# Kernel tuning notes

Measured on AMD Instinct MI355X. Metric: run time of the kernel, lower is better.

Reference implementation:

```python
import jax, jax.numpy as jnp
import numpy as np
from jax import lax

D_MODEL = 512
D_STATE = 64
D_CONV = 4
EXPAND = 2
HEADDIM = 64
D_INNER = EXPAND * D_MODEL          # 1024
NHEADS = D_INNER // HEADDIM         # 16
CONV_DIM = D_INNER + 2 * D_STATE    # 1152 (x, B, C go through depthwise conv)
D_PROJ = 2 * D_INNER + 2 * D_STATE + NHEADS  # 2192
EPS = 1e-5


def silu(x):
    return x * jax.nn.sigmoid(x)


def layernorm(x, w, b):
    mu = jnp.mean(x, axis=-1, keepdims=True)
    var = jnp.mean((x - mu) ** 2, axis=-1, keepdims=True)
    return (x - mu) * lax.rsqrt(var + EPS) * w + b


def mamba2(x, in_w, conv_w, conv_b, dt_bias, A_log, D_h, mnorm_w, out_w):
    """Faithful Mamba2 forward (sequential selective-scan form of SSD).
    x: [B, L, D_MODEL]"""
    Bsz, L, _ = x.shape
    zxbcdt = x @ in_w  # [B, L, D_PROJ]
    z = zxbcdt[..., :D_INNER]
    xBC = zxbcdt[..., D_INNER:D_INNER + CONV_DIM]
    dt = zxbcdt[..., -NHEADS:]

    # causal depthwise conv1d over sequence, then SiLU
    xBC_pad = jnp.pad(xBC, ((0, 0), (D_CONV - 1, 0), (0, 0)))
    xBC = lax.conv_general_dilated(
        xBC_pad, conv_w, window_strides=(1,), padding='VALID',
        dimension_numbers=('NWC', 'WIO', 'NWC'), feature_group_count=CONV_DIM)
    xBC = silu(xBC + conv_b)

    xh = xBC[..., :D_INNER].reshape(Bsz, L, NHEADS, HEADDIM)      # [B,L,H,P]
    Bc = xBC[..., D_INNER:D_INNER + D_STATE]                      # [B,L,N]
    Cc = xBC[..., D_INNER + D_STATE:]                             # [B,L,N]

    dt = jax.nn.softplus(dt + dt_bias)          # [B,L,H]
    dA = jnp.exp(dt * (-jnp.exp(A_log)))        # [B,L,H]
    dtx = dt[..., None] * xh                    # [B,L,H,P]

    def step(h, ins):
        dA_t, dtx_t, B_t, C_t = ins  # [B,H], [B,H,P], [B,N], [B,N]
        h = h * dA_t[:, :, None, None] + dtx_t[..., None] * B_t[:, None, None, :]
        y = jnp.einsum('bhpn,bn->bhp', h, C_t)
        return h, y

    h0 = jnp.zeros((Bsz, NHEADS, HEADDIM, D_STATE), x.dtype)
    xs = (jnp.moveaxis(dA, 1, 0), jnp.moveaxis(dtx, 1, 0),
          jnp.moveaxis(Bc, 1, 0), jnp.moveaxis(Cc, 1, 0))
    _, ys = lax.scan(step, h0, xs)              # [L,B,H,P]
    y = jnp.moveaxis(ys, 0, 1) + D_h[None, None, :, None] * xh
    y = y.reshape(Bsz, L, D_INNER)

    # gated RMSNorm: rmsnorm(y * silu(z)) * weight
    g = y * silu(z)
    g = g * lax.rsqrt(jnp.mean(g * g, axis=-1, keepdims=True) + EPS) * mnorm_w
    return g @ out_w  # [B, L, D_MODEL]


def setup_inputs() -> dict:
    key = jax.random.key(0)
    ks = jax.random.split(key, 16)
    B, L = 2, 4096
    s = 0.02
    inp = {
        'x': jax.random.normal(ks[0], (B, L, D_MODEL), jnp.float32),
        'norm_in_w': jnp.ones((D_MODEL,), jnp.float32),
        'norm_in_b': jnp.zeros((D_MODEL,), jnp.float32),
        'norm_out_w': jnp.ones((D_MODEL,), jnp.float32),
        'norm_out_b': jnp.zeros((D_MODEL,), jnp.float32),
        'in_w': jax.random.normal(ks[1], (D_MODEL, D_PROJ), jnp.float32) * s,
        'conv_w': jax.random.normal(ks[2], (D_CONV, 1, CONV_DIM), jnp.float32) * 0.1,
        'conv_b': jnp.zeros((CONV_DIM,), jnp.float32),
        'dt_bias': jnp.log(jnp.expm1(jax.random.uniform(ks[3], (NHEADS,), jnp.float32, 0.001, 0.1))),
        'A_log': jnp.log(jnp.arange(1, NHEADS + 1, dtype=jnp.float32)),
        'D_h': jnp.ones((NHEADS,), jnp.float32),
        'mnorm_w': jnp.ones((D_INNER,), jnp.float32),
        'out_w': jax.random.normal(ks[4], (D_INNER, D_MODEL), jnp.float32) * s,
        'ff_w1': jax.random.normal(ks[5], (D_MODEL, 4 * D_MODEL), jnp.float32) * s,
        'ff_b1': jnp.zeros((4 * D_MODEL,), jnp.float32),
        'ff_w2': jax.random.normal(ks[6], (4 * D_MODEL, D_MODEL), jnp.float32) * s,
        'ff_b2': jnp.zeros((D_MODEL,), jnp.float32),
    }
    return inp


def reference(x, norm_in_w, norm_in_b, norm_out_w, norm_out_b, in_w, conv_w,
              conv_b, dt_bias, A_log, D_h, mnorm_w, out_w, ff_w1, ff_b1,
              ff_w2, ff_b2):
    xn = layernorm(x, norm_in_w, norm_in_b)
    fwd = mamba2(xn, in_w, conv_w, conv_b, dt_bias, A_log, D_h, mnorm_w, out_w)
    bwd = mamba2(jnp.flip(xn, axis=1), in_w, conv_w, conv_b, dt_bias, A_log,
                 D_h, mnorm_w, out_w)
    m = layernorm(fwd + jnp.flip(bwd, axis=1), norm_out_w, norm_out_b)
    ff = jax.nn.gelu(m @ ff_w1 + ff_b1, approximate=False) @ ff_w2 + ff_b2
    return ff + x
```

## Files before the change

### kernel.cpp

```cpp
#include <hip/hip_runtime.h>
#include <hip/hip_bf16.h>

#define LSEQ 4096
#define BSZ 2
#define DMODEL 512
#define DINNER 1024
#define DSTATE 64
#define NHEADS 16
#define CONVDIM 1152
#define DPROJ 2192
#define NPAD 2304
#define NTOK (BSZ*LSEQ)
#define NCH 64

typedef __attribute__((ext_vector_type(8))) short short8;
typedef __attribute__((ext_vector_type(4))) float f32x4;

__device__ inline unsigned short f2b(float v){
  unsigned int u = __builtin_bit_cast(unsigned int, v);
  unsigned int r = (u + 0x7FFFu + ((u >> 16) & 1u)) >> 16;
  return (unsigned short)r;
}
__device__ inline float b2f(unsigned short u){
  unsigned int x = ((unsigned int)u) << 16;
  return __builtin_bit_cast(float, x);
}
__device__ inline uint4 pack8(const float* v){
  uint4 pk;
  pk.x = (unsigned)f2b(v[0]) | ((unsigned)f2b(v[1])<<16);
  pk.y = (unsigned)f2b(v[2]) | ((unsigned)f2b(v[3])<<16);
  pk.z = (unsigned)f2b(v[4]) | ((unsigned)f2b(v[5])<<16);
  pk.w = (unsigned)f2b(v[6]) | ((unsigned)f2b(v[7])<<16);
  return pk;
}
__device__ inline float gelu_f(float x){
  float x2 = x*x;
  float u = x*(0.7978845608f + 0.0356774081f*x2);
  float au = fabsf(u);
  float z = __expf(-2.f*au);
  float t = (1.f - z)/(1.f + z);
  t = (u >= 0.f) ? t : -t;
  return 0.5f*x*(1.f + t);
}

#define GLL16(gp, lp) __builtin_amdgcn_global_load_lds( \
    (const __attribute__((address_space(1))) unsigned int*)(gp), \
    (__attribute__((address_space(3))) unsigned int*)(lp), 16, 0, 0)

__global__ __launch_bounds__(256) void wconv_t(const float* __restrict__ src,
    unsigned short* __restrict__ dst, int K, int Nsrc, int Npad){
  __shared__ float t[32][33];
  int n0 = blockIdx.x*32, k0 = blockIdx.y*32;
  int tx = threadIdx.x & 31, ty = threadIdx.x >> 5;
  for (int i=0;i<4;i++){
    int k = k0 + ty + i*8; int n = n0 + tx;
    t[ty + i*8][tx] = (n < Nsrc) ? src[(size_t)k*Nsrc + n] : 0.f;
  }
  __syncthreads();
  for (int i=0;i<4;i++){
    int n = n0 + ty + i*8; int k = k0 + tx;
    if (n < Npad) dst[(size_t)n*K + k] = f2b(t[tx][ty + i*8]);
  }
}

__global__ __launch_bounds__(256) void layernorm_k(const float* __restrict__ in,
    const float* __restrict__ w, const float* __restrict__ bb, unsigned short* __restrict__ out){
  int row = blockIdx.x; int tid = threadIdx.x;
  const float* r = in + (size_t)row*DMODEL;
  float v0 = r[tid], v1 = r[tid+256];
  float s = v0+v1, sq = v0*v0+v1*v1;
  for (int m=32;m>=1;m>>=1){ s += __shfl_xor(s,m); sq += __shfl_xor(sq,m); }
  __shared__ float ws_[4], wq_[4];
  int wave = tid>>6, lane = tid&63;
  if (lane==0){ ws_[wave]=s; wq_[wave]=sq; }
  __syncthreads();
  s = ws_[0]+ws_[1]+ws_[2]+ws_[3]; sq = wq_[0]+wq_[1]+wq_[2]+wq_[3];
  float mu = s * (1.f/DMODEL);
  float var = sq * (1.f/DMODEL) - mu*mu;
  float rs = rsqrtf(var + 1e-5f);
  out[(size_t)row*DMODEL + tid]     = f2b((v0-mu)*rs*w[tid] + bb[tid]);
  out[(size_t)row*DMODEL + tid+256] = f2b((v1-mu)*rs*w[tid+256] + bb[tid+256]);
}

__global__ __launch_bounds__(256) void layernorm2_k(const float* __restrict__ in0,
    const float* __restrict__ in1,
    const float* __restrict__ w, const float* __restrict__ bb, unsigned short* __restrict__ out){
  int row = blockIdx.x; int tid = threadIdx.x;
  const float* r0 = in0 + (size_t)row*DMODEL;
  const float* r1 = in1 + (size_t)row*DMODEL;
  float v0 = r0[tid] + r1[tid], v1 = r0[tid+256] + r1[tid+256];
  float s = v0+v1, sq = v0*v0+v1*v1;
  for (int m=32;m>=1;m>>=1){ s += __shfl_xor(s,m); sq += __shfl_xor(sq,m); }
  __shared__ float ws_[4], wq_[4];
  int wave = tid>>6, lane = tid&63;
  if (lane==0){ ws_[wave]=s; wq_[wave]=sq; }
  __syncthreads();
  s = ws_[0]+ws_[1]+ws_[2]+ws_[3]; sq = wq_[0]+wq_[1]+wq_[2]+wq_[3];
  float mu = s * (1.f/DMODEL);
  float var = sq * (1.f/DMODEL) - mu*mu;
  float rs = rsqrtf(var + 1e-5f);
  out[(size_t)row*DMODEL + tid]     = f2b((v0-mu)*rs*w[tid] + bb[tid]);
  out[(size_t)row*DMODEL + tid+256] = f2b((v1-mu)*rs*w[tid+256] + bb[tid+256]);
}

__global__ __launch_bounds__(256) void reduce4_k(const float* __restrict__ pa,
    const float* __restrict__ pb, const float* __restrict__ bias,
    const float* __restrict__ resid, float* __restrict__ out){
  const size_t MN4 = (size_t)NTOK*DMODEL/4;
  for (size_t i = (size_t)blockIdx.x*256 + threadIdx.x; i < MN4; i += (size_t)gridDim.x*256){
    float4 a0 = ((const float4*)pa)[i];
    float4 a1 = ((const float4*)pa)[i + MN4];
    float4 b0 = ((const float4*)pb)[i];
    float4 b1 = ((const float4*)pb)[i + MN4];
    float4 rv = ((const float4*)resid)[i];
    int col = (int)((i*4) & (DMODEL-1));
    const float4 bs = *(const float4*)(bias + col);
    float4 o;
    o.x = a0.x + a1.x + b0.x + b1.x + bs.x + rv.x;
    o.y = a0.y + a1.y + b0.y + b1.y + bs.y + rv.y;
    o.z = a0.z + a1.z + b0.z + b1.z + bs.z + rv.z;
    o.w = a0.w + a1.w + b0.w + b1.w + bs.w + rv.w;
    ((float4*)out)[i] = o;
  }
}

__global__ __launch_bounds__(512, 2) void gemm256_k(const unsigned short* __restrict__ A,
    const unsigned short* __restrict__ Bt, void* __restrict__ outp, void* __restrict__ outp_hi,
    int M, int N, int K, int klen, int epi, const float* __restrict__ bias){
  __shared__ __align__(16) unsigned short As[32768];
  __shared__ __align__(16) unsigned short Bs[32768];
  const int tid = threadIdx.x;
  const int lane = tid & 63, wave = tid >> 6;
  const int wr = wave >> 2, wc = wave & 3;
  const int l15 = lane & 15, q = lane >> 4;
  int nbx = gridDim.x;
  int bid = blockIdx.y * nbx + blockIdx.x;
  int cpx = (nbx * gridDim.y) >> 3;
  int swz = (bid & 7) * cpx + (bid >> 3);
  int bn = swz % nbx, bm = swz / nbx;
  const int kstart = blockIdx.z * klen;
  const int NT = klen >> 6;
  const int j0 = tid, j1 = tid + 512;
  const int rr0 = j0 >> 2, rr1 = j1 >> 2;
  const int sc0 = (j0 & 3) ^ ((rr0 >> 1) & 3);
  const int sc1 = (j1 & 3) ^ ((rr1 >> 1) & 3);
  const unsigned short* a0 = A  + (size_t)(bm*256 + rr0)*K + kstart + sc0*8;
  const unsigned short* a1 = A  + (size_t)(bm*256 + rr1)*K + kstart + sc1*8;
  const unsigned short* b0 = Bt + (size_t)(bn*256 + rr0)*K + kstart + sc0*8;
  const unsigned short* b1 = Bt + (size_t)(bn*256 + rr1)*K + kstart + sc1*8;
  unsigned short* lA0 = As + j0*8;
  unsigned short* lA1 = As + j1*8;
  unsigned short* lB0 = Bs + j0*8;
  unsigned short* lB1 = Bs + j1*8;
#define STGA(t,kh) { const int go=(t)*64+(kh)*32, lo=((t)&1)*16384+(kh)*8192; \
  GLL16(a0+go, lA0+lo); GLL16(a1+go, lA1+lo); }
#define STGB(t,kh) { const int go=(t)*64+(kh)*32, lo=((t)&1)*16384+(kh)*8192; \
  GLL16(b0+go, lB0+lo); GLL16(b1+go, lB1+lo); }
  f32x4 acc[8][4];
  #pragma unroll
  for (int i=0;i<8;i++)
    #pragma unroll
    for (int j=0;j<4;j++) acc[i][j] = (f32x4){0.f,0.f,0.f,0.f};
  STGA(0,0); STGB(0,0); STGA(0,1); STGB(0,1);
  STGA(1,0); STGB(1,0);
  asm volatile("s_waitcnt vmcnt(4)" ::: "memory");
  __builtin_amdgcn_s_barrier();
  const int cOfs = (q ^ ((l15 >> 1) & 3)) * 8;
  const int arow = wr*128 + l15;
  const int brow = wc*64  + l15;
  for (int t = 0; t < NT; ++t){
    const unsigned short* Ab = As + (t & 1)*16384;
    const unsigned short* Bb = Bs + (t & 1)*16384;
    short8 af[4], bf4[4];
    #pragma unroll
    for (int mi=0;mi<4;mi++) af[mi]  = *(const short8*)(Ab + (arow + mi*16)*32 + cOfs);
    #pragma unroll
    for (int nt=0;nt<4;nt++) bf4[nt] = *(const short8*)(Bb + (brow + nt*16)*32 + cOfs);
    if (t+1 < NT) STGA(t+1,1);
    __builtin_amdgcn_s_barrier();
    asm volatile("s_waitcnt lgkmcnt(0)" ::: "memory");
    __builtin_amdgcn_sched_barrier(0);
    __builtin_amdgcn_s_setprio(1);
    #pragma unroll
    for (int mi=0;mi<4;mi++)
      #pragma unroll
      for (int nt=0;nt<4;nt++)
        acc[mi][nt] = __builtin_amdgcn_mfma_f32_16x16x32_bf16(af[mi], bf4[nt], acc[mi][nt], 0,0,0);
    __builtin_amdgcn_s_setprio(0);
    __builtin_amdgcn_s_barrier();
    #pragma unroll
    for (int mi=0;mi<4;mi++) af[mi] = *(const short8*)(Ab + (arow + (4+mi)*16)*32 + cOfs);
    if (t+1 < NT) STGB(t+1,1);
    __builtin_amdgcn_s_barrier();
    asm volatile("s_waitcnt lgkmcnt(0)" ::: "memory");
    __builtin_amdgcn_sched_barrier(0);
    __builtin_amdgcn_s_setprio(1);
    #pragma unroll
    for (int mi=0;mi<4;mi++)
      #pragma unroll
      for (int nt=0;nt<4;nt++)
        acc[4+mi][nt] = __builtin_amdgcn_mfma_f32_16x16x32_bf16(af[mi], bf4[nt], acc[4+mi][nt], 0,0,0);
    __builtin_amdgcn_s_setprio(0);
    __builtin_amdgcn_s_barrier();
    #pragma unroll
    for (int mi=0;mi<4;mi++) af[mi]  = *(const short8*)(Ab + 8192 + (arow + mi*16)*32 + cOfs);
    #pragma unroll
    for (int nt=0;nt<4;nt++) bf4[nt] = *(const short8*)(Bb + 8192 + (brow + nt*16)*32 + cOfs);
    if (t+2 < NT) STGA(t+2,0);
    __builtin_amdgcn_s_barrier();
    asm volatile("s_waitcnt lgkmcnt(0)" ::: "memory");
    __builtin_amdgcn_sched_barrier(0);
    __builtin_amdgcn_s_setprio(1);
    #pragma unroll
    for (int mi=0;mi<4;mi++)
      #pragma unroll
      for (int nt=0;nt<4;nt++)
        acc[mi][nt] = __builtin_amdgcn_mfma_f32_16x16x32_bf16(af[mi], bf4[nt], acc[mi][nt], 0,0,0);
    __builtin_amdgcn_s_setprio(0);
    __builtin_amdgcn_s_barrier();
    #pragma unroll
    for (int mi=0;mi<4;mi++) af[mi] = *(const short8*)(Ab + 8192 + (arow + (4+mi)*16)*32 + cOfs);
    if (t+2 < NT) STGB(t+2,0);
    __builtin_amdgcn_s_barrier();
    asm volatile("s_waitcnt lgkmcnt(0)" ::: "memory");
    __builtin_amdgcn_sched_barrier(0);
    __builtin_amdgcn_s_setprio(1);
    #pragma unroll
    for (int mi=0;mi<4;mi++)
      #pragma unroll
      for (int nt=0;nt<4;nt++)
        acc[4+mi][nt] = __builtin_amdgcn_mfma_f32_16x16x32_bf16(af[mi], bf4[nt], acc[4+mi][nt], 0,0,0);
    __builtin_amdgcn_s_setprio(0);
    if (t+2 < NT)      { asm volatile("s_waitcnt vmcnt(4)" ::: "memory"); }
    else if (t+1 < NT) { asm volatile("s_waitcnt vmcnt(0)" ::: "memory"); }
    __builtin_amdgcn_s_barrier();
  }
#undef STGA
#undef STGB
  float* cb = (float*)As + wave*1040;
  const int rbase = q*4;
  const int gr0t = bm*256 + wr*128;
  const int gc0 = bn*256 + wc*64;
  #pragma unroll
  for (int mt=0; mt<8; mt++){
    #pragma unroll
    for (int nt=0;nt<4;nt++)
      #pragma unroll
      for (int r=0;r<4;r++)
        cb[(rbase+r)*65 + nt*16 + l15] = acc[mt][nt][r];
    int gr0 = gr0t + mt*16;
    if (epi == 0){
      float* po = (float*)((blockIdx.z < 2) ? outp : outp_hi)
                + (size_t)(blockIdx.z & 1) * ((size_t)M * N);
      int r4 = lane >> 4, c0f = (lane & 15)*4;
      #pragma unroll
      for (int h=0; h<4; h++){
        int row = h*4 + r4;
        float4 v;
        v.x = cb[row*65 + c0f + 0];
        v.y = cb[row*65 + c0f + 1];
        v.z = cb[row*65 + c0f + 2];
        v.w = cb[row*65 + c0f + 3];
        *(float4*)(po + (size_t)(gr0+row)*N + gc0 + c0f) = v;
      }
    } else {
      int r8 = lane >> 3, c0 = (lane & 7)*8;
      #pragma unroll
      for (int h=0; h<2; h++){
        int row = h*8 + r8;
        float v[8];
        #pragma unroll
        for (int u=0;u<8;u++) v[u] = cb[row*65 + c0 + u];
        if (epi == 1){
          #pragma unroll
          for (int u=0;u<8;u++) v[u] = gelu_f(v[u] + bias[gc0 + c0 + u]);
        }
        *(uint4*)((unsigned short*)outp + (size_t)(gr0+row)*N + gc0 + c0) = pack8(v);
      }
    }
  }
}

__global__ __launch_bounds__(256) void dt_k(const unsigned short* __restrict__ zx,
    const float* __restrict__ dt_bias, const float* __restrict__ A_log,
    float* __restrict__ dAb, float* __restrict__ dtb){
  int b = blockIdx.y;
  int t = blockIdx.x*16 + (threadIdx.x>>4);
  int h = threadIdx.x & 15;
  float raw = b2f(zx[((size_t)b*LSEQ + t)*NPAD + (DINNER+CONVDIM) + h]) + dt_bias[h];
  float dt = (raw > 20.f) ? raw : log1pf(expf(raw));
  float dA = expf(-expf(A_log[h]) * dt);
  size_t f = ((size_t)b*LSEQ + t)*NHEADS + h;
  size_t r = ((size_t)(BSZ+b)*LSEQ + (LSEQ-1-t))*NHEADS + h;
  dAb[f] = dA; dtb[f] = dt;
  dAb[r] = dA; dtb[r] = dt;
}

__global__ __launch_bounds__(256) void conv_x_k(const unsigned short* __restrict__ zx,
    const float* __restrict__ conv_w, const float* __restrict__ conv_b,
    const float* __restrict__ dtb, unsigned short* __restrict__ dtxb,
    unsigned short* __restrict__ zcomp){
  int b = blockIdx.y;
  int t0blk = blockIdx.x * 32;
  int tid = threadIdx.x;
  int half = tid >> 7, cg = tid & 127;
  int c0 = cg * 8;
  int head = c0 >> 6;
  float wk[4][8], bias8[8];
  #pragma unroll
  for (int k=0;k<4;k++)
    #pragma unroll
    for (int j=0;j<8;j++) wk[k][j] = conv_w[k*CONVDIM + c0 + j];
  #pragma unroll
  for (int j=0;j<8;j++) bias8[j] = conv_b[c0 + j];
  __shared__ float sdtf[32][16], sdtb[32][16];
  for (int r = tid; r < 512; r += 256){
    int i = r >> 4, h = r & 15;
    sdtf[i][h] = dtb[((size_t)b*LSEQ + t0blk + i)*NHEADS + h];
    sdtb[i][h] = dtb[((size_t)(BSZ+b)*LSEQ + (LSEQ-1-(t0blk+i)))*NHEADS + h];
  }
  __syncthreads();
  int t0 = t0blk + half*16;
  float w0[8],w1[8],w2[8],w3[8];
  #pragma unroll
  for (int j=0;j<8;j++){ w1[j]=0.f; w2[j]=0.f; w3[j]=0.f; }
  for (int it=0; it<22; ++it){
    int t = t0 - 3 + it;
    #pragma unroll
    for (int j=0;j<8;j++){ w0[j]=w1[j]; w1[j]=w2[j]; w2[j]=w3[j]; }
    if (t >= 0 && t < LSEQ){
      uint4 xv = *(const uint4*)(zx + ((size_t)b*LSEQ + t)*NPAD + DINNER + c0);
      const unsigned short* xs = (const unsigned short*)&xv;
      #pragma unroll
      for (int j=0;j<8;j++) w3[j] = b2f(xs[j]);
      if (t >= t0 && t < t0+16){
        uint4 zv = *(const uint4*)(zx + ((size_t)b*LSEQ + t)*NPAD + c0);
        *(uint4*)(zcomp + ((size_t)b*LSEQ + t)*DINNER + c0) = zv;
      }
    } else {
      #pragma unroll
      for (int j=0;j<8;j++) w3[j] = 0.f;
    }
    if (t >= t0 && t < t0+16){
      float dtf = sdtf[t - t0blk][head];
      float v[8];
      #pragma unroll
      for (int j=0;j<8;j++){
        float a = bias8[j] + wk[0][j]*w0[j] + wk[1][j]*w1[j] + wk[2][j]*w2[j] + wk[3][j]*w3[j];
        v[j] = (a / (1.f + __expf(-a))) * dtf;
      }
      *(uint4*)(dtxb + ((size_t)b*LSEQ + t)*DINNER + c0) = pack8(v);
    }
    int tau = t - 3;
    if (tau >= t0 && tau < t0+16){
      float dtv = sdtb[tau - t0blk][head];
      float v[8];
      #pragma unroll
      for (int j=0;j<8;j++){
        float a = bias8[j] + wk[0][j]*w3[j] + wk[1][j]*w2[j] + wk[2][j]*w1[j] + wk[3][j]*w0[j];
        v[j] = (a / (1.f + __expf(-a))) * dtv;
      }
      *(uint4*)(dtxb + ((size_t)(BSZ+b)*LSEQ + (LSEQ-1-tau))*DINNER + c0) = pack8(v);
    }
  }
}

__global__ __launch_bounds__(256) void conv_bc_k(const unsigned short* __restrict__ zx,
    const float* __restrict__ conv_w, const float* __restrict__ conv_b,
    unsigned short* __restrict__ Bb, unsigned short* __restrict__ Cb){
  int b = blockIdx.y;
  int t0blk = blockIdx.x * 64;
  int tid = threadIdx.x;
  int slot = tid >> 4, cg = tid & 15;
  int c0 = cg*8;
  int ccol = DINNER + 1024 + c0;
  int cw = 1024 + c0;
  float wk[4][8], bias8[8];
  #pragma unroll
  for (int k=0;k<4;k++)
    #pragma unroll
    for (int j=0;j<8;j++) wk[k][j] = conv_w[k*CONVDIM + cw + j];
  #pragma unroll
  for (int j=0;j<8;j++) bias8[j] = conv_b[cw + j];
  int t0 = t0blk + slot*4;
  float w0[8],w1[8],w2[8],w3[8];
  #pragma unroll
  for (int j=0;j<8;j++){ w1[j]=0.f; w2[j]=0.f; w3[j]=0.f; }
  for (int it=0; it<10; ++it){
    int t = t0 - 3 + it;
    #pragma unroll
    for (int j=0;j<8;j++){ w0[j]=w1[j]; w1[j]=w2[j]; w2[j]=w3[j]; }
    if (t >= 0 && t < LSEQ){
      uint4 xv = *(const uint4*)(zx + ((size_t)b*LSEQ + t)*NPAD + ccol);
      const unsigned short* xs = (const unsigned short*)&xv;
      #pragma unroll
      for (int j=0;j<8;j++) w3[j] = b2f(xs[j]);
    } else {
      #pragma unroll
      for (int j=0;j<8;j++) w3[j] = 0.f;
    }
    if (t >= t0 && t < t0+4){
      float v[8];
      #pragma unroll
      for (int j=0;j<8;j++){
        float a = bias8[j] + wk[0][j]*w0[j] + wk[1][j]*w1[j] + wk[2][j]*w2[j] + wk[3][j]*w3[j];
        v[j] = a / (1.f + __expf(-a));
      }
      size_t tok = (size_t)b*LSEQ + t;
      if (c0 < 64) *(uint4*)(Bb + tok*DSTATE + c0)      = pack8(v);
      else         *(uint4*)(Cb + tok*DSTATE + (c0-64)) = pack8(v);
    }
    int tau = t - 3;
    if (tau >= t0 && tau < t0+4){
      float v[8];
      #pragma unroll
      for (int j=0;j<8;j++){
        float a = bias8[j] + wk[0][j]*w3[j] + wk[1][j]*w2[j] + wk[2][j]*w1[j] + wk[3][j]*w0[j];
        v[j] = a / (1.f + __expf(-a));
      }
      size_t tok = (size_t)(BSZ+b)*LSEQ + (LSEQ-1-tau);
      if (c0 < 64) *(uint4*)(Bb + tok*DSTATE + c0)      = pack8(v);
      else         *(uint4*)(Cb + tok*DSTATE + (c0-64)) = pack8(v);
    }
  }
}

template<int SA, int SB>
__device__ inline void gemm64s(const unsigned short* Ab, const unsigned short* Bb_,
                               int l15, int q, f32x4 acc[4][4]){
  #pragma unroll
  for (int ks=0; ks<2; ks++){
    short8 af[4], bf4[4];
    #pragma unroll
    for (int mt=0;mt<4;mt++){
      int r = mt*16 + l15;
      int c = ks*4 + q; if (SA) c ^= (r>>3)&7;
      af[mt] = *(const short8*)(Ab + r*72 + c*8);
    }
    #pragma unroll
    for (int nt=0;nt<4;nt++){
      int r = nt*16 + l15;
      int c = ks*4 + q; if (SB) c ^= (r>>3)&7;
      bf4[nt] = *(const short8*)(Bb_ + r*72 + c*8);
    }
    #pragma unroll
    for (int mt=0;mt<4;mt++)
      #pragma unroll
      for (int nt=0;nt<4;nt++)
        acc[mt][nt] = __builtin_amdgcn_mfma_f32_16x16x32_bf16(af[mt], bf4[nt], acc[mt][nt], 0,0,0);
  }
}
__device__ inline void gemm64(const unsigned short* Ab, const unsigned short* Bb_,
                              int l15, int q, f32x4 acc[4][4]){
  gemm64s<0,0>(Ab, Bb_, l15, q, acc);
}

__global__ __launch_bounds__(64) void ssd1_k(const float* __restrict__ dAb,
    const unsigned short* __restrict__ dtxb, const unsigned short* __restrict__ Bb,
    const unsigned short* __restrict__ Cb,
    unsigned short* __restrict__ y0, unsigned short* __restrict__ y1,
    unsigned short* __restrict__ hbuf, float* __restrict__ Pch, float* __restrict__ ebuf){
  int ch = blockIdx.x, h = blockIdx.y, z = blockIdx.z;
  int d = z >> 1, b = z & 1;
  int lane = threadIdx.x;
  int l15 = lane & 15, q = lane >> 4;
  int tr = lane >> 3, cb8 = (lane & 7)*8;
  int m7 = lane & 7;
  size_t tokb = (size_t)z*LSEQ + (size_t)ch*64;
  size_t zhc = ((size_t)z*NHEADS + h)*NCH + ch;
  __shared__ __align__(16) unsigned short S1[64*72];
  __shared__ __align__(16) unsigned short S2[64*72];
  __shared__ __align__(16) unsigned short S3[64*72];
  __shared__ float Lb[64];
  float L = fmaxf(logf(dAb[(tokb + lane)*NHEADS + h]), -60.f);
  #pragma unroll
  for (int off=1; off<64; off<<=1){
    float v = __shfl_up(L, off);
    if (lane >= off) L += v;
  }
  Lb[lane] = L;
  float e = __expf(L);
  ebuf[zhc*64 + lane] = e;
  if (lane == 63) Pch[zhc] = e;
  for (int i=0;i<8;i++){
    int t = i*8 + tr;
    *(uint4*)&S1[t*72 + cb8] = *(const uint4*)(Cb + (tokb+t)*DSTATE + cb8);
    *(uint4*)&S2[t*72 + cb8] = *(const uint4*)(Bb + (tokb+t)*DSTATE + cb8);
    uint4 xv = *(const uint4*)(dtxb + (tokb+t)*DINNER + (size_t)h*64 + cb8);
    const unsigned short* xs = (const unsigned short*)&xv;
    int csw = ((i ^ m7) << 3) + tr;
    #pragma unroll
    for (int j=0;j<8;j++) S3[(cb8+j)*72 + csw] = xs[j];
  }
  f32x4 sa[4][4];
  for (int i=0;i<4;i++) for (int j=0;j<4;j++) sa[i][j] = (f32x4){0.f,0.f,0.f,0.f};
  gemm64s<0,0>(S1, S2, l15, q, sa);
  float Lsv[4];
  #pragma unroll
  for (int nt=0;nt<4;nt++) Lsv[nt] = Lb[nt*16 + l15];
  int sch = l15 >> 3, sin = l15 & 7;
  #pragma unroll
  for (int mt=0;mt<4;mt++){
    #pragma unroll
    for (int r=0;r<4;r++){
      int t = mt*16 + q*4 + r;
      int trow = (t>>3)&7;
      float Lt = Lb[t];
      #pragma unroll
      for (int nt=0;nt<4;nt++){
        int s = nt*16 + l15;
        float v = (t >= s) ? __expf(Lt - Lsv[nt]) * sa[mt][nt][r] : 0.f;
        S1[t*72 + (((nt*2 + sch) ^ trow)<<3) + sin] = f2b(v);
      }
    }
  }
  f32x4 ya[4][4];
  for (int i=0;i<4;i++) for (int j=0;j<4;j++) ya[i][j] = (f32x4){0.f,0.f,0.f,0.f};
  gemm64s<1,1>(S1, S3, l15, q, ya);
  #pragma unroll
  for (int mt=0;mt<4;mt++)
    #pragma unroll
    for (int pt=0;pt<4;pt++)
      #pragma unroll
      for (int r=0;r<4;r++)
        S2[(mt*16+q*4+r)*72 + pt*16 + l15] = f2b(ya[mt][pt][r]);
  unsigned short* yb = d ? y1 : y0;
  for (int i=0;i<8;i++){
    int t = i*8 + tr; int g = ch*64 + t;
    int tph = d ? (LSEQ-1-g) : g;
    *(uint4*)(yb + ((size_t)b*LSEQ + tph)*DINNER + (size_t)h*64 + cb8) = *(uint4*)&S2[t*72 + cb8];
  }
  float L63 = Lb[63];
  for (int i=0;i<8;i++){
    int s = i*8 + tr;
    float w = __expf(L63 - Lb[s]);
    uint4 bv = *(const uint4*)(Bb + (tokb+s)*DSTATE + cb8);
    const unsigned short* bs = (const unsigned short*)&bv;
    int csw = ((i ^ m7) << 3) + tr;
    #pragma unroll
    for (int j=0;j<8;j++) S2[(cb8+j)*72 + csw] = f2b(w * b2f(bs[j]));
  }
  f32x4 ga[4][4];
  for (int i=0;i<4;i++) for (int j=0;j<4;j++) ga[i][j] = (f32x4){0.f,0.f,0.f,0.f};
  gemm64s<1,1>(S3, S2, l15, q, ga);
  #pragma unroll
  for (int pt=0;pt<4;pt++)
    #pragma unroll
    for (int nt=0;nt<4;nt++)
      #pragma unroll
      for (int r=0;r<4;r++)
        S1[(pt*16+q*4+r)*72 + nt*16 + l15] = f2b(ga[pt][nt][r]);
  for (int i=0;i<8;i++){
    int p = i*8 + tr;
    *(uint4*)(hbuf + zhc*4096 + (size_t)p*64 + cb8) = *(uint4*)&S1[p*72 + cb8];
  }
}

__global__ __launch_bounds__(256) void comb_k(unsigned short* __restrict__ hbuf,
    const float* __restrict__ Pch){
  int u = blockIdx.x; int tid = threadIdx.x;
  int kb = blockIdx.y * 4;
  size_t base0 = ((size_t)u*NCH)*4096;
  float hreg[4];
  unsigned short ccur[4], cnxt[4] = {0,0,0,0};
  #pragma unroll
  for (int k=0;k<4;k++){ hreg[k]=0.f; ccur[k] = hbuf[base0 + tid + (size_t)(kb+k)*256]; }
  float Pc = Pch[(size_t)u*NCH], Pn = 0.f;
  for (int ch=0; ch<NCH; ch++){
    size_t base = base0 + (size_t)ch*4096;
    if (ch+1 < NCH){
      size_t bnx = base + 4096;
      #pragma unroll
      for (int k=0;k<4;k++) cnxt[k] = hbuf[bnx + tid + (size_t)(kb+k)*256];
      Pn = Pch[(size_t)u*NCH + ch + 1];
    }
    #pragma unroll
    for (int k=0;k<4;k++){
      hbuf[base + tid + (size_t)(kb+k)*256] = f2b(hreg[k]);
      hreg[k] = hreg[k]*Pc + b2f(ccur[k]);
    }
    #pragma unroll
    for (int k=0;k<4;k++) ccur[k] = cnxt[k];
    Pc = Pn;
  }
}

__global__ __launch_bounds__(64) void ssd2_k(const unsigned short* __restrict__ Cb,
    const unsigned short* __restrict__ hbuf, const unsigned short* __restrict__ dtxb,
    const float* __restrict__ dtb, const float* __restrict__ ebuf, const float* __restrict__ Dh,
    unsigned short* __restrict__ y0, unsigned short* __restrict__ y1){
  int ch = blockIdx.x, h = blockIdx.y, z = blockIdx.z;
  int d = z >> 1, b = z & 1;
  int lane = threadIdx.x;
  int l15 = lane & 15, q = lane >> 4;
  int tr = lane >> 3, cb8 = (lane & 7)*8;
  size_t tokb = (size_t)z*LSEQ + (size_t)ch*64;
  size_t zhc = ((size_t)z*NHEADS + h)*NCH + ch;
  __shared__ __align__(16) unsigned short S1[64*72];
  __shared__ __align__(16) unsigned short S2[64*72];
  __shared__ __align__(16) unsigned short S3[64*72];
  __shared__ float eb2[64], dti[64];
  eb2[lane] = ebuf[zhc*64 + lane];
  dti[lane] = 1.f / dtb[(tokb + lane)*NHEADS + h];
  float Dv = Dh[h];
  for (int i=0;i<8;i++){
    int t = i*8 + tr;
    *(uint4*)&S1[t*72 + cb8] = *(const uint4*)(Cb + (tokb+t)*DSTATE + cb8);
    *(uint4*)&S2[t*72 + cb8] = *(const uint4*)(hbuf + zhc*4096 + (size_t)t*64 + cb8);
  }
  f32x4 acc[4][4];
  for (int i=0;i<4;i++) for (int j=0;j<4;j++) acc[i][j] = (f32x4){0.f,0.f,0.f,0.f};
  gemm64(S1, S2, l15, q, acc);
  unsigned short* yb = d ? y1 : y0;
  #pragma unroll
  for (int mt=0;mt<4;mt++){
    #pragma unroll
    for (int r=0;r<4;r++){
      int t = mt*16 + q*4 + r; int g = ch*64 + t;
      int tph = d ? (LSEQ-1-g) : g;
      size_t rowb = ((size_t)b*LSEQ + tph)*DINNER + (size_t)h*64;
      size_t dxb_ = (tokb + t)*DINNER + (size_t)h*64;
      float et = eb2[t], di = dti[t];
      #pragma unroll
      for (int pt=0;pt<4;pt++){
        int p = pt*16 + l15;
        float v = acc[mt][pt][r]*et + b2f(yb[rowb + p]) + Dv * b2f(dtxb[dxb_ + p]) * di;
        S3[t*72 + p] = f2b(v);
      }
    }
  }
  for (int i=0;i<8;i++){
    int t = i*8 + tr; int g = ch*64 + t;
    int tph = d ? (LSEQ-1-g) : g;
    *(uint4*)(yb + ((size_t)b*LSEQ + tph)*DINNER + (size_t)h*64 + cb8) = *(uint4*)&S3[t*72 + cb8];
  }
}

__global__ __launch_bounds__(256) void gate_k(const unsigned short* __restrict__ y0,
    const unsigned short* __restrict__ y1, const unsigned short* __restrict__ zcomp,
    const float* __restrict__ mnw, unsigned short* __restrict__ gsum){
  int tok = blockIdx.x; int tid = threadIdx.x;
  __shared__ float g0s[DINNER], g1s[DINNER];
  float ss0 = 0.f, ss1 = 0.f;
  for (int i=0;i<4;i++){
    int c = tid + i*256;
    float z = b2f(zcomp[(size_t)tok*DINNER + c]);
    float sz = z / (1.f + __expf(-z));
    float g0 = b2f(y0[(size_t)tok*DINNER + c]) * sz;
    float g1 = b2f(y1[(size_t)tok*DINNER + c]) * sz;
    g0s[c] = g0; g1s[c] = g1;
    ss0 += g0*g0; ss1 += g1*g1;
  }
  for (int m=32;m>=1;m>>=1){ ss0 += __shfl_xor(ss0,m); ss1 += __shfl_xor(ss1,m); }
  __shared__ float w0[4], w1[4];
  int wave = tid>>6, lane = tid&63;
  if (lane==0){ w0[wave]=ss0; w1[wave]=ss1; }
  __syncthreads();
  ss0 = w0[0]+w0[1]+w0[2]+w0[3];
  ss1 = w1[0]+w1[1]+w1[2]+w1[3];
  float r0 = rsqrtf(ss0*(1.f/DINNER) + 1e-5f);
  float r1 = rsqrtf(ss1*(1.f/DINNER) + 1e-5f);
  for (int i=0;i<4;i++){
    int c = tid + i*256;
    gsum[(size_t)tok*DINNER + c] = f2b((g0s[c]*r0 + g1s[c]*r1) * mnw[c]);
  }
}

extern "C" void kernel_launch(void* const* d_in, const int* in_sizes, int n_in,
                              void* d_out, int out_size, void* d_ws, size_t ws_size,
                              hipStream_t stream){
  const float* x       = (const float*)d_in[0];
  const float* nin_w   = (const float*)d_in[1];
  const float* nin_b   = (const float*)d_in[2];
  const float* nout_w  = (const float*)d_in[3];
  const float* nout_b  = (const float*)d_in[4];
  const float* in_w    = (const float*)d_in[5];
  const float* conv_w  = (const float*)d_in[6];
  const float* conv_b  = (const float*)d_in[7];
  const float* dt_bias = (const float*)d_in[8];
  const float* A_log   = (const float*)d_in[9];
  const float* D_h     = (const float*)d_in[10];
  const float* mnorm_w = (const float*)d_in[11];
  const float* out_w   = (const float*)d_in[12];
  const float* ff_w1   = (const float*)d_in[13];
  const float* ff_b1   = (const float*)d_in[14];
  const float* ff_w2   = (const float*)d_in[15];
  const float* ff_b2   = (const float*)d_in[16];
  float* out = (float*)d_out;

  char* ws = (char*)d_ws;
  size_t off = 0;
  auto alloc = [&](size_t bytes)->char*{
    char* p = ws + off; off = (off + bytes + 255) & ~(size_t)255; return p; };
  unsigned short* xn_bf = (unsigned short*)alloc((size_t)NTOK*DMODEL*2);
  unsigned short* in_wT = (unsigned short*)alloc((size_t)NPAD*DMODEL*2);
  unsigned short* out_wT= (unsigned short*)alloc((size_t)DMODEL*DINNER*2);
  unsigned short* w1T   = (unsigned short*)alloc((size_t)2048*DMODEL*2);
  unsigned short* w2T   = (unsigned short*)alloc((size_t)DMODEL*2048*2);
  unsigned short* zx    = (unsigned short*)alloc((size_t)NTOK*NPAD*2);
  unsigned short* zcomp = (unsigned short*)alloc((size_t)NTOK*DINNER*2);
  float*          dAb   = (float*)alloc((size_t)2*NTOK*NHEADS*4);
  float*          dtb   = (float*)alloc((size_t)2*NTOK*NHEADS*4);
  unsigned short* Bb    = (unsigned short*)alloc((size_t)2*NTOK*DSTATE*2);
  unsigned short* Cb    = (unsigned short*)alloc((size_t)2*NTOK*DSTATE*2);
  unsigned short* dtxb  = (unsigned short*)alloc((size_t)2*NTOK*DINNER*2);
  unsigned short* y0    = (unsigned short*)alloc((size_t)NTOK*DINNER*2);
  unsigned short* y1    = (unsigned short*)alloc((size_t)NTOK*DINNER*2);
  float*          Pch   = (float*)alloc((size_t)64*NCH*4);
  float*          ebuf  = (float*)alloc((size_t)64*NCH*64*4);
  size_t need = off;
  if (need > ws_size) return;

  unsigned short* hbuf  = zx;
  unsigned short* gsum  = dtxb;
  unsigned short* m_bf  = y0;
  unsigned short* h1    = zx;
  float* mp   = (float*)zx;
  float* fp01 = (float*)dtxb;
  float* fp23 = (float*)y0;

  wconv_t<<<dim3(NPAD/32,   DMODEL/32), 256, 0, stream>>>(in_w,  in_wT,  DMODEL, DPROJ,  NPAD);
  wconv_t<<<dim3(DMODEL/32, DINNER/32), 256, 0, stream>>>(out_w, out_wT, DINNER, DMODEL, DMODEL);
  wconv_t<<<dim3(2048/32,   DMODEL/32), 256, 0, stream>>>(ff_w1, w1T,    DMODEL, 2048,   2048);
  wconv_t<<<dim3(DMODEL/32, 2048/32),   256, 0, stream>>>(ff_w2, w2T,    2048,   DMODEL, DMODEL);
  layernorm_k<<<NTOK, 256, 0, stream>>>(x, nin_w, nin_b, xn_bf);
  gemm256_k<<<dim3(NPAD/256, NTOK/256, 1), 512, 0, stream>>>(xn_bf, in_wT, zx, nullptr, NTOK, NPAD, DMODEL, DMODEL, 3, nullptr);
  dt_k<<<dim3(LSEQ/16, BSZ), 256, 0, stream>>>(zx, dt_bias, A_log, dAb, dtb);
  conv_x_k<<<dim3(LSEQ/32, BSZ), 256, 0, stream>>>(zx, conv_w, conv_b, dtb, dtxb, zcomp);
  conv_bc_k<<<dim3(LSEQ/64, BSZ), 256, 0, stream>>>(zx, conv_w, conv_b, Bb, Cb);
  ssd1_k<<<dim3(NCH, NHEADS, 2*BSZ), 64, 0, stream>>>(dAb, dtxb, Bb, Cb, y0, y1, hbuf, Pch, ebuf);
  comb_k<<<dim3(64, 4), 256, 0, stream>>>(hbuf, Pch);
  ssd2_k<<<dim3(NCH, NHEADS, 2*BSZ), 64, 0, stream>>>(Cb, hbuf, dtxb, dtb, ebuf, D_h, y0, y1);
  gate_k<<<NTOK, 256, 0, stream>>>(y0, y1, zcomp, mnorm_w, gsum);
  gemm256_k<<<dim3(DMODEL/256, NTOK/256, 2), 512, 0, stream>>>(gsum, out_wT, mp, nullptr, NTOK, DMODEL, DINNER, 512, 0, nullptr);
  layernorm2_k<<<NTOK, 256, 0, stream>>>(mp, mp + (size_t)NTOK*DMODEL, nout_w, nout_b, m_bf);
  gemm256_k<<<dim3(2048/256, NTOK/256, 1), 512, 0, stream>>>(m_bf, w1T, h1, nullptr, NTOK, 2048, DMODEL, DMODEL, 1, ff_b1);
  gemm256_k<<<dim3(DMODEL/256, NTOK/256, 4), 512, 0, stream>>>(h1, w2T, fp01, fp23, NTOK, DMODEL, 2048, 512, 0, nullptr);
  reduce4_k<<<2048, 256, 0, stream>>>(fp01, fp23, ff_b2, x, out);
}
```

Measured before the change: 403.1 us.

## Software-pipeline LDS fragment loads with register double-buffering in GEMM main loop

Restructures the bf16 MFMA GEMM inner loop so LDS fragment reads for the next quarter-step go into separate register buffers (a0f/a1f/b0f/b1f) while the current MFMAs run. Most per-quarter barriers and explicit lgkmcnt(0) waits are removed, and the first fragments of the next k-tile are prefetched right after the end-of-iteration barrier. The aim is to hide LDS latency and cut synchronisation stalls. In exchange it raises register pressure and changes the vmcnt bookkeeping, which risks races on the double-buffered LDS tiles or lower occupancy.

```diff
diff --git a/kernel.cpp b/kernel.cpp
--- a/kernel.cpp
+++ b/kernel.cpp
@@ -165,71 +165,70 @@
   STGA(1,0); STGB(1,0);
   asm volatile("s_waitcnt vmcnt(4)" ::: "memory");
   __builtin_amdgcn_s_barrier();
+  __builtin_amdgcn_sched_barrier(0);
   const int cOfs = (q ^ ((l15 >> 1) & 3)) * 8;
   const int arow = wr*128 + l15;
   const int brow = wc*64  + l15;
+  short8 a0f[4], a1f[4], b0f[4], b1f[4];
+  #pragma unroll
+  for (int mi=0;mi<4;mi++) a0f[mi] = *(const short8*)(As + (arow + mi*16)*32 + cOfs);
+  #pragma unroll
+  for (int nt=0;nt<4;nt++) b0f[nt] = *(const short8*)(Bs + (brow + nt*16)*32 + cOfs);
   for (int t = 0; t < NT; ++t){
-    const unsigned short* Ab = As + (t & 1)*16384;
-    const unsigned short* Bb = Bs + (t & 1)*16384;
-    short8 af[4], bf4[4];
-    #pragma unroll
-    for (int mi=0;mi<4;mi++) af[mi]  = *(const short8*)(Ab + (arow + mi*16)*32 + cOfs);
-    #pragma unroll
-    for (int nt=0;nt<4;nt++) bf4[nt] = *(const short8*)(Bb + (brow + nt*16)*32 + cOfs);
+    const unsigned short* Ab  = As + (t & 1)*16384;
+    const unsigned short* Bb  = Bs + (t & 1)*16384;
+    const unsigned short* Abn = As + ((~t) & 1)*16384;
+    const unsigned short* Bbn = Bs + ((~t) & 1)*16384;
+    #pragma unroll
+    for (int mi=0;mi<4;mi++) a1f[mi] = *(const short8*)(Ab + (arow + (4+mi)*16)*32 + cOfs);
     if (t+1 < NT) STGA(t+1,1);
-    __builtin_amdgcn_s_barrier();
-    asm volatile("s_waitcnt lgkmcnt(0)" ::: "memory");
-    __builtin_amdgcn_sched_barrier(0);
     __builtin_amdgcn_s_setprio(1);
     #pragma unroll
     for (int mi=0;mi<4;mi++)
       #pragma unroll
       for (int nt=0;nt<4;nt++)
-        acc[mi][nt] = __builtin_amdgcn_mfma_f32_16x16x32_bf16(af[mi], bf4[nt], acc[mi][nt], 0,0,0);
+        acc[mi][nt] = __builtin_amdgcn_mfma_f32_16x16x32_bf16(a0f[mi], b0f[nt], acc[mi][nt], 0,0,0);
+    __builtin_amdgcn_s_setprio(0);
+    #pragma unroll
+    for (int mi=0;mi<4;mi++) a0f[mi] = *(const short8*)(Ab + 8192 + (arow + mi*16)*32 + cOfs);
+    #pragma unroll
+    for (int nt=0;nt<4;nt++) b1f[nt] = *(const short8*)(Bb + 8192 + (brow + nt*16)*32 + cOfs);
+    if (t+1 < NT) STGB(t+1,1);
+    __builtin_amdgcn_s_setprio(1);
+    #pragma unroll
+    for (int mi=0;mi<4;mi++)
+      #pragma unroll
+      for (int nt=0;nt<4;nt++)
+        acc[4+mi][nt] = __builtin_amdgcn_mfma_f32_16x16x32_bf16(a1f[mi], b0f[nt], acc[4+mi][nt], 0,0,0);
     __builtin_amdgcn_s_setprio(0);
     __builtin_amdgcn_s_barrier();
     #pragma unroll
-    for (int mi=0;mi<4;mi++) af[mi] = *(const short8*)(Ab + (arow + (4+mi)*16)*32 + cOfs);
-    if (t+1 < NT) STGB(t+1,1);
+    for (int mi=0;mi<4;mi++) a1f[mi] = *(const short8*)(Ab + 8192 + (arow + (4+mi)*16)*32 + cOfs);
+    if (t+2 < NT) STGA(t+2,0);
+    __builtin_amdgcn_s_setprio(1);
+    #pragma unroll
+    for (int mi=0;mi<4;mi++)
+      #pragma unroll
+      for (int nt=0;nt<4;nt++)
+        acc[mi][nt] = __builtin_amdgcn_mfma_f32_16x16x32_bf16(a0f[mi], b1f[nt], acc[mi][nt], 0,0,0);
+    __builtin_amdgcn_s_setprio(0);
+    if (t+2 < NT) STGB(t+2,0);
+    if (t+2 < NT)      { asm volatile("s_waitcnt vmcnt(8)" ::: "memory"); }
+    else if (t+1 < NT) { asm volatile("s_waitcnt vmcnt(4)" ::: "memory"); }
     __builtin_amdgcn_s_barrier();
-    asm volatile("s_waitcnt lgkmcnt(0)" ::: "memory");
     __builtin_amdgcn_sched_barrier(0);
+    if (t+1 < NT){
+      #pragma unroll
+      for (int mi=0;mi<4;mi++) a0f[mi] = *(const short8*)(Abn + (arow + mi*16)*32 + cOfs);
+      #pragma unroll
+      for (int nt=0;nt<4;nt++) b0f[nt] = *(const short8*)(Bbn + (brow + nt*16)*32 + cOfs);
+    }
     __builtin_amdgcn_s_setprio(1);
     #pragma unroll
     for (int mi=0;mi<4;mi++)
       #pragma unroll
       for (int nt=0;nt<4;nt++)
-        acc[4+mi][nt] = __builtin_amdgcn_mfma_f32_16x16x32_bf16(af[mi], bf4[nt], acc[4+mi][nt], 0,0,0);
-    __builtin_amdgcn_s_setprio(0);
-    __builtin_amdgcn_s_barrier();
-    #pragma unroll
-    for (int mi=0;mi<4;mi++) af[mi]  = *(const short8*)(Ab + 8192 + (arow + mi*16)*32 + cOfs);
-    #pragma unroll
-    for (int nt=0;nt<4;nt++) bf4[nt] = *(const short8*)(Bb + 8192 + (brow + nt*16)*32 + cOfs);
-    if (t+2 < NT) STGA(t+2,0);
-    __builtin_amdgcn_s_barrier();
-    asm volatile("s_waitcnt lgkmcnt(0)" ::: "memory");
-    __builtin_amdgcn_sched_barrier(0);
-    __builtin_amdgcn_s_setprio(1);
-    #pragma unroll
-    for (int mi=0;mi<4;mi++)
-      #pragma unroll
-      for (int nt=0;nt<4;nt++)
-        acc[mi][nt] = __builtin_amdgcn_mfma_f32_16x16x32_bf16(af[mi], bf4[nt], acc[mi][nt], 0,0,0);
-    __builtin_amdgcn_s_setprio(0);
-    __builtin_amdgcn_s_barrier();
-    #pragma unroll
-    for (int mi=0;mi<4;mi++) af[mi] = *(const short8*)(Ab + 8192 + (arow + (4+mi)*16)*32 + cOfs);
-    if (t+2 < NT) STGB(t+2,0);
-    __builtin_amdgcn_s_barrier();
-    asm volatile("s_waitcnt lgkmcnt(0)" ::: "memory");
-    __builtin_amdgcn_sched_barrier(0);
-    __builtin_amdgcn_s_setprio(1);
-    #pragma unroll
-    for (int mi=0;mi<4;mi++)
-      #pragma unroll
-      for (int nt=0;nt<4;nt++)
-        acc[4+mi][nt] = __builtin_amdgcn_mfma_f32_16x16x32_bf16(af[mi], bf4[nt], acc[4+mi][nt], 0,0,0);
+        acc[4+mi][nt] = __builtin_amdgcn_mfma_f32_16x16x32_bf16(a1f[mi], b1f[nt], acc[4+mi][nt], 0,0,0);
     __builtin_amdgcn_s_setprio(0);
     if (t+2 < NT)      { asm volatile("s_waitcnt vmcnt(4)" ::: "memory"); }
     else if (t+1 < NT) { asm volatile("s_waitcnt vmcnt(0)" ::: "memory"); }
```

Result: no change. 403.7 us (+0.2%).

## Shrink GEMM tile to 128x256 with simpler double-buffered K=32 pipeline

Applied to the files above, without the earlier changes.

Replaces the 256x256 GEMM kernel with a 128x256 tile that steps K by 32, uses a single-stage double-buffered load per iteration and a smaller LDS footprint, and raises launch bounds to allow more resident blocks. All four GEMMs now launch twice as many blocks. The out-projection GEMM switches to a 4-way split-K, so its layernorm now sums four partials. The aim is better occupancy and more blocks to fill the GPU's CUs, at the cost of less data reuse per tile and more frequent barriers.

```diff
diff --git a/kernel.cpp b/kernel.cpp
--- a/kernel.cpp
+++ b/kernel.cpp
@@ -82,13 +82,13 @@
   out[(size_t)row*DMODEL + tid+256] = f2b((v1-mu)*rs*w[tid+256] + bb[tid+256]);
 }
 
-__global__ __launch_bounds__(256) void layernorm2_k(const float* __restrict__ in0,
-    const float* __restrict__ in1,
+__global__ __launch_bounds__(256) void layernorm4_k(const float* __restrict__ in0,
+    const float* __restrict__ in1, const float* __restrict__ in2, const float* __restrict__ in3,
     const float* __restrict__ w, const float* __restrict__ bb, unsigned short* __restrict__ out){
   int row = blockIdx.x; int tid = threadIdx.x;
-  const float* r0 = in0 + (size_t)row*DMODEL;
-  const float* r1 = in1 + (size_t)row*DMODEL;
-  float v0 = r0[tid] + r1[tid], v1 = r0[tid+256] + r1[tid+256];
+  size_t o = (size_t)row*DMODEL;
+  float v0 = in0[o+tid] + in1[o+tid] + in2[o+tid] + in3[o+tid];
+  float v1 = in0[o+tid+256] + in1[o+tid+256] + in2[o+tid+256] + in3[o+tid+256];
   float s = v0+v1, sq = v0*v0+v1*v1;
   for (int m=32;m>=1;m>>=1){ s += __shfl_xor(s,m); sq += __shfl_xor(sq,m); }
   __shared__ float ws_[4], wq_[4];
@@ -99,8 +99,8 @@
   float mu = s * (1.f/DMODEL);
   float var = sq * (1.f/DMODEL) - mu*mu;
   float rs = rsqrtf(var + 1e-5f);
-  out[(size_t)row*DMODEL + tid]     = f2b((v0-mu)*rs*w[tid] + bb[tid]);
-  out[(size_t)row*DMODEL + tid+256] = f2b((v1-mu)*rs*w[tid+256] + bb[tid+256]);
+  out[o + tid]     = f2b((v0-mu)*rs*w[tid] + bb[tid]);
+  out[o + tid+256] = f2b((v1-mu)*rs*w[tid+256] + bb[tid+256]);
 }
 
 __global__ __launch_bounds__(256) void reduce4_k(const float* __restrict__ pa,
@@ -124,11 +124,12 @@
   }
 }
 
-__global__ __launch_bounds__(512, 2) void gemm256_k(const unsigned short* __restrict__ A,
+__global__ __launch_bounds__(512, 4) void gemm128_k(const unsigned short* __restrict__ A,
     const unsigned short* __restrict__ Bt, void* __restrict__ outp, void* __restrict__ outp_hi,
     int M, int N, int K, int klen, int epi, const float* __restrict__ bias){
-  __shared__ __align__(16) unsigned short As[32768];
-  __shared__ __align__(16) unsigned short Bs[32768];
+  __shared__ __align__(16) unsigned short sm[24576];
+  unsigned short* As = sm;
+  unsigned short* Bs = sm + 8192;
   const int tid = threadIdx.x;
   const int lane = tid & 63, wave = tid >> 6;
   const int wr = wave >> 2, wc = wave & 3;
@@ -139,110 +140,57 @@
   int swz = (bid & 7) * cpx + (bid >> 3);
   int bn = swz % nbx, bm = swz / nbx;
   const int kstart = blockIdx.z * klen;
-  const int NT = klen >> 6;
-  const int j0 = tid, j1 = tid + 512;
-  const int rr0 = j0 >> 2, rr1 = j1 >> 2;
-  const int sc0 = (j0 & 3) ^ ((rr0 >> 1) & 3);
-  const int sc1 = (j1 & 3) ^ ((rr1 >> 1) & 3);
-  const unsigned short* a0 = A  + (size_t)(bm*256 + rr0)*K + kstart + sc0*8;
-  const unsigned short* a1 = A  + (size_t)(bm*256 + rr1)*K + kstart + sc1*8;
-  const unsigned short* b0 = Bt + (size_t)(bn*256 + rr0)*K + kstart + sc0*8;
-  const unsigned short* b1 = Bt + (size_t)(bn*256 + rr1)*K + kstart + sc1*8;
-  unsigned short* lA0 = As + j0*8;
-  unsigned short* lA1 = As + j1*8;
-  unsigned short* lB0 = Bs + j0*8;
-  unsigned short* lB1 = Bs + j1*8;
-#define STGA(t,kh) { const int go=(t)*64+(kh)*32, lo=((t)&1)*16384+(kh)*8192; \
-  GLL16(a0+go, lA0+lo); GLL16(a1+go, lA1+lo); }
-#define STGB(t,kh) { const int go=(t)*64+(kh)*32, lo=((t)&1)*16384+(kh)*8192; \
-  GLL16(b0+go, lB0+lo); GLL16(b1+go, lB1+lo); }
-  f32x4 acc[8][4];
-  #pragma unroll
-  for (int i=0;i<8;i++)
+  const int NT = klen >> 5;
+  const int ra  = tid >> 2;
+  const int sca = (tid & 3) ^ ((ra >> 1) & 3);
+  const int jb1 = tid + 512;
+  const int rb1 = jb1 >> 2;
+  const int scb1 = (jb1 & 3) ^ ((rb1 >> 1) & 3);
+  const unsigned short* ga  = A  + (size_t)(bm*128 + ra )*K + kstart + sca*8;
+  const unsigned short* gb0 = Bt + (size_t)(bn*256 + ra )*K + kstart + sca*8;
+  const unsigned short* gb1 = Bt + (size_t)(bn*256 + rb1)*K + kstart + scb1*8;
+  unsigned short* lAa = As + tid*8;
+  unsigned short* lB0 = Bs + tid*8;
+  unsigned short* lB1 = Bs + jb1*8;
+#define STG(t) { const int go=(t)*32, loa=((t)&1)*4096, lob=((t)&1)*8192; \
+  GLL16(ga+go, lAa+loa); GLL16(gb0+go, lB0+lob); GLL16(gb1+go, lB1+lob); }
+  f32x4 acc[4][4];
+  #pragma unroll
+  for (int i=0;i<4;i++)
     #pragma unroll
     for (int j=0;j<4;j++) acc[i][j] = (f32x4){0.f,0.f,0.f,0.f};
-  STGA(0,0); STGB(0,0); STGA(0,1); STGB(0,1);
-  STGA(1,0); STGB(1,0);
-  asm volatile("s_waitcnt vmcnt(4)" ::: "memory");
-  __builtin_amdgcn_s_barrier();
+  STG(0); STG(1);
   const int cOfs = (q ^ ((l15 >> 1) & 3)) * 8;
-  const int arow = wr*128 + l15;
-  const int brow = wc*64  + l15;
+  const int arow = wr*64 + l15;
+  const int brow = wc*64 + l15;
   for (int t = 0; t < NT; ++t){
-    const unsigned short* Ab = As + (t & 1)*16384;
-    const unsigned short* Bb = Bs + (t & 1)*16384;
+    if (t+1 < NT) { asm volatile("s_waitcnt vmcnt(3)" ::: "memory"); }
+    else          { asm volatile("s_waitcnt vmcnt(0)" ::: "memory"); }
+    __builtin_amdgcn_s_barrier();
+    const unsigned short* Ab = As + (t & 1)*4096;
+    const unsigned short* Bb = Bs + (t & 1)*8192;
     short8 af[4], bf4[4];
     #pragma unroll
-    for (int mi=0;mi<4;mi++) af[mi]  = *(const short8*)(Ab + (arow + mi*16)*32 + cOfs);
+    for (int mt=0;mt<4;mt++) af[mt]  = *(const short8*)(Ab + (arow + mt*16)*32 + cOfs);
     #pragma unroll
     for (int nt=0;nt<4;nt++) bf4[nt] = *(const short8*)(Bb + (brow + nt*16)*32 + cOfs);
-    if (t+1 < NT) STGA(t+1,1);
-    __builtin_amdgcn_s_barrier();
-    asm volatile("s_waitcnt lgkmcnt(0)" ::: "memory");
-    __builtin_amdgcn_sched_barrier(0);
     __builtin_amdgcn_s_setprio(1);
     #pragma unroll
-    for (int mi=0;mi<4;mi++)
+    for (int mt=0;mt<4;mt++)
       #pragma unroll
       for (int nt=0;nt<4;nt++)
-        acc[mi][nt] = __builtin_amdgcn_mfma_f32_16x16x32_bf16(af[mi], bf4[nt], acc[mi][nt], 0,0,0);
+        acc[mt][nt] = __builtin_amdgcn_mfma_f32_16x16x32_bf16(af[mt], bf4[nt], acc[mt][nt], 0,0,0);
     __builtin_amdgcn_s_setprio(0);
     __builtin_amdgcn_s_barrier();
-    #pragma unroll
-    for (int mi=0;mi<4;mi++) af[mi] = *(const short8*)(Ab + (arow + (4+mi)*16)*32 + cOfs);
-    if (t+1 < NT) STGB(t+1,1);
-    __builtin_amdgcn_s_barrier();
-    asm volatile("s_waitcnt lgkmcnt(0)" ::: "memory");
-    __builtin_amdgcn_sched_barrier(0);
-    __builtin_amdgcn_s_setprio(1);
-    #pragma unroll
-    for (int mi=0;mi<4;mi++)
-      #pragma unroll
-      for (int nt=0;nt<4;nt++)
-        acc[4+mi][nt] = __builtin_amdgcn_mfma_f32_16x16x32_bf16(af[mi], bf4[nt], acc[4+mi][nt], 0,0,0);
-    __builtin_amdgcn_s_setprio(0);
-    __builtin_amdgcn_s_barrier();
-    #pragma unroll
-    for (int mi=0;mi<4;mi++) af[mi]  = *(const short8*)(Ab + 8192 + (arow + mi*16)*32 + cOfs);
-    #pragma unroll
-    for (int nt=0;nt<4;nt++) bf4[nt] = *(const short8*)(Bb + 8192 + (brow + nt*16)*32 + cOfs);
-    if (t+2 < NT) STGA(t+2,0);
-    __builtin_amdgcn_s_barrier();
-    asm volatile("s_waitcnt lgkmcnt(0)" ::: "memory");
-    __builtin_amdgcn_sched_barrier(0);
-    __builtin_amdgcn_s_setprio(1);
-    #pragma unroll
-    for (int mi=0;mi<4;mi++)
-      #pragma unroll
-      for (int nt=0;nt<4;nt++)
-        acc[mi][nt] = __builtin_amdgcn_mfma_f32_16x16x32_bf16(af[mi], bf4[nt], acc[mi][nt], 0,0,0);
-    __builtin_amdgcn_s_setprio(0);
-    __builtin_amdgcn_s_barrier();
-    #pragma unroll
-    for (int mi=0;mi<4;mi++) af[mi] = *(const short8*)(Ab + 8192 + (arow + (4+mi)*16)*32 + cOfs);
-    if (t+2 < NT) STGB(t+2,0);
-    __builtin_amdgcn_s_barrier();
-    asm volatile("s_waitcnt lgkmcnt(0)" ::: "memory");
-    __builtin_amdgcn_sched_barrier(0);
-    __builtin_amdgcn_s_setprio(1);
-    #pragma unroll
-    for (int mi=0;mi<4;mi++)
-      #pragma unroll
-      for (int nt=0;nt<4;nt++)
-        acc[4+mi][nt] = __builtin_amdgcn_mfma_f32_16x16x32_bf16(af[mi], bf4[nt], acc[4+mi][nt], 0,0,0);
-    __builtin_amdgcn_s_setprio(0);
-    if (t+2 < NT)      { asm volatile("s_waitcnt vmcnt(4)" ::: "memory"); }
-    else if (t+1 < NT) { asm volatile("s_waitcnt vmcnt(0)" ::: "memory"); }
-    __builtin_amdgcn_s_barrier();
-  }
-#undef STGA
-#undef STGB
-  float* cb = (float*)As + wave*1040;
+    if (t+2 < NT) STG(t+2);
+  }
+#undef STG
+  float* cb = (float*)sm + wave*1040;
   const int rbase = q*4;
-  const int gr0t = bm*256 + wr*128;
+  const int gr0t = bm*128 + wr*64;
   const int gc0 = bn*256 + wc*64;
   #pragma unroll
-  for (int mt=0; mt<8; mt++){
+  for (int mt=0; mt<4; mt++){
     #pragma unroll
     for (int nt=0;nt<4;nt++)
       #pragma unroll
@@ -713,9 +661,10 @@
 
   unsigned short* hbuf  = zx;
   unsigned short* gsum  = dtxb;
-  unsigned short* m_bf  = y0;
+  float* mp01 = (float*)zx;
+  float* mp23 = (float*)y0;
+  unsigned short* m_bf  = xn_bf;
   unsigned short* h1    = zx;
-  float* mp   = (float*)zx;
   float* fp01 = (float*)dtxb;
   float* fp23 = (float*)y0;
 
@@ -724,7 +673,7 @@
   wconv_t<<<dim3(2048/32,   DMODEL/32), 256, 0, stream>>>(ff_w1, w1T,    DMODEL, 2048,   2048);
   wconv_t<<<dim3(DMODEL/32, 2048/32),   256, 0, stream>>>(ff_w2, w2T,    2048,   DMODEL, DMODEL);
   layernorm_k<<<NTOK, 256, 0, stream>>>(x, nin_w, nin_b, xn_bf);
-  gemm256_k<<<dim3(NPAD/256, NTOK/256, 1), 512, 0, stream>>>(xn_bf, in_wT, zx, nullptr, NTOK, NPAD, DMODEL, DMODEL, 3, nullptr);
+  gemm128_k<<<dim3(NPAD/256, NTOK/128, 1), 512, 0, stream>>>(xn_bf, in_wT, zx, nullptr, NTOK, NPAD, DMODEL, DMODEL, 3, nullptr);
   dt_k<<<dim3(LSEQ/16, BSZ), 256, 0, stream>>>(zx, dt_bias, A_log, dAb, dtb);
   conv_x_k<<<dim3(LSEQ/32, BSZ), 256, 0, stream>>>(zx, conv_w, conv_b, dtb, dtxb, zcomp);
   conv_bc_k<<<dim3(LSEQ/64, BSZ), 256, 0, stream>>>(zx, conv_w, conv_b, Bb, Cb);
@@ -732,9 +681,9 @@
   comb_k<<<dim3(64, 4), 256, 0, stream>>>(hbuf, Pch);
   ssd2_k<<<dim3(NCH, NHEADS, 2*BSZ), 64, 0, stream>>>(Cb, hbuf, dtxb, dtb, ebuf, D_h, y0, y1);
   gate_k<<<NTOK, 256, 0, stream>>>(y0, y1, zcomp, mnorm_w, gsum);
-  gemm256_k<<<dim3(DMODEL/256, NTOK/256, 2), 512, 0, stream>>>(gsum, out_wT, mp, nullptr, NTOK, DMODEL, DINNER, 512, 0, nullptr);
-  layernorm2_k<<<NTOK, 256, 0, stream>>>(mp, mp + (size_t)NTOK*DMODEL, nout_w, nout_b, m_bf);
-  gemm256_k<<<dim3(2048/256, NTOK/256, 1), 512, 0, stream>>>(m_bf, w1T, h1, nullptr, NTOK, 2048, DMODEL, DMODEL, 1, ff_b1);
-  gemm256_k<<<dim3(DMODEL/256, NTOK/256, 4), 512, 0, stream>>>(h1, w2T, fp01, fp23, NTOK, DMODEL, 2048, 512, 0, nullptr);
+  gemm128_k<<<dim3(DMODEL/256, NTOK/128, 4), 512, 0, stream>>>(gsum, out_wT, mp01, mp23, NTOK, DMODEL, DINNER, 256, 0, nullptr);
+  layernorm4_k<<<NTOK, 256, 0, stream>>>(mp01, mp01 + (size_t)NTOK*DMODEL, mp23, mp23 + (size_t)NTOK*DMODEL, nout_w, nout_b, m_bf);
+  gemm128_k<<<dim3(2048/256, NTOK/128, 1), 512, 0, stream>>>(m_bf, w1T, h1, nullptr, NTOK, 2048, DMODEL, DMODEL, 1, ff_b1);
+  gemm128_k<<<dim3(DMODEL/256, NTOK/128, 4), 512, 0, stream>>>(h1, w2T, fp01, fp23, NTOK, DMODEL, 2048, 512, 0, nullptr);
   reduce4_k<<<2048, 256, 0, stream>>>(fp01, fp23, ff_b2, x, out);
 }
```

Result: no change. 398.7 us (-1.1%).
